# Kernel tuning notes

Measured on AMD Instinct MI355X. Metric: run time of the kernel, lower is better.

The kernel has to match this reference:

```python
import jax, jax.numpy as jnp
import numpy as np

B, N1, N2 = 16, 196, 196
C1, C2, H, O = 768, 768, 512, 128


def setup_inputs() -> dict:
    key = jax.random.key(0)
    k1, k2, kw1, kw2, kwp, kbp = jax.random.split(key, 6)
    x1 = jax.random.normal(k1, (B, N1, C1), dtype=jnp.float32)
    x2 = jax.random.normal(k2, (B, N2, C2), dtype=jnp.float32)
    # kaiming-uniform-ish init scale
    W1 = jax.random.uniform(kw1, (C1, H), dtype=jnp.float32, minval=-1, maxval=1) * np.sqrt(3.0 / C1)
    W2 = jax.random.uniform(kw2, (C2, H), dtype=jnp.float32, minval=-1, maxval=1) * np.sqrt(3.0 / C2)
    Wp = jax.random.uniform(kwp, (H, O), dtype=jnp.float32, minval=-1, maxval=1) * np.sqrt(3.0 / H)
    bp = jax.random.uniform(kbp, (O,), dtype=jnp.float32, minval=-1, maxval=1) * (1.0 / np.sqrt(H))
    return {"x1": x1, "x2": x2, "W1": W1, "W2": W2, "Wp": Wp, "bp": bp}


def reference(x1, x2, W1, W2, Wp, bp):
    # x1: [B,N1,C1], x2: [B,N2,C2]
    h1 = jax.nn.relu(jnp.einsum('bnc,ch->bnh', x1, W1))  # [B,N1,H]
    h2 = jax.nn.relu(jnp.einsum('bmc,ch->bmh', x2, W2))  # [B,N2,H]
    # Original: ((h1[:,:,None,:] * h2[:,None,:,:]) @ Wp + bp).sum(dim=(1,2)).
    # Mathematically identical fused form: sum_{i,j} h1[b,i,h]*h2[b,j,h]
    #   = (sum_i h1)[b,h] * (sum_j h2)[b,h]; bias accumulates N1*N2 times.
    s = h1.sum(axis=1) * h2.sum(axis=1)                   # [B,H]
    return jnp.einsum('bh,ho->bo', s, Wp) + bp * (N1 * N2)
```

## Files before the change

kernel.cpp:

```cpp
#include <hip/hip_runtime.h>
#include <hip/hip_bf16.h>


#define NB 16
#define NROW 196
#define KC_ 768
#define HH 512
#define OO 128

using short8 = __attribute__((ext_vector_type(8))) short;
using f32x16 = __attribute__((ext_vector_type(16))) float;

__device__ __forceinline__ short2 pk2bf(float a, float b) {
    __hip_bfloat162 h = __float22bfloat162_rn(make_float2(a, b));
    union { __hip_bfloat162 h; short2 s; } u; u.h = h;
    return u.s;
}

__global__ __launch_bounds__(512, 1)
void gemm_relu_rowsum(const float* __restrict__ x1, const float* __restrict__ x2,
                      const float* __restrict__ W1, const float* __restrict__ W2,
                      float* __restrict__ sbuf) {
    __shared__ unsigned short Alds[2][8 * 128 * 8];
    __shared__ unsigned short Blds[2][8 * 128 * 8];
    __shared__ float psum[16 * 32];

    const int bid = blockIdx.x;
    const int p  = bid & 31;
    const int tt = bid >> 5;
    const int branch = p >> 4;
    const int b      = p & 15;
    const int ht = tt >> 1;
    const int mh = tt & 1;
    const int c0 = ht * 128;

    const float* __restrict__ x = branch ? x2 : x1;
    const float* __restrict__ W = branch ? W2 : W1;

    const int t  = threadIdx.x;
    const int rn = t & 127;
    const int kg = t >> 7;

    const int r_abs = mh * 128 + rn;
    const bool valid = r_abs < NROW;
    const float* xrow  = x + (b * NROW + (valid ? r_abs : 0)) * KC_ + kg * 16;
    const float* Wbase = W + c0 + rn;

    float4 av[4];
    float  bv[2][8];

    auto load_stage = [&](int kc) {
        const int k0 = kc * 64;
        if (valid) {
#pragma unroll
            for (int i = 0; i < 4; ++i)
                av[i] = *(const float4*)(xrow + k0 + 4 * i);
        } else {
#pragma unroll
            for (int i = 0; i < 4; ++i) av[i] = make_float4(0.f, 0.f, 0.f, 0.f);
        }
#pragma unroll
        for (int u = 0; u < 2; ++u)
#pragma unroll
            for (int j = 0; j < 8; ++j)
                bv[u][j] = Wbase[(k0 + (kg + 4 * u) * 8 + j) * HH];
    };

    auto write_stage = [&](int buf) {
        short8 w0, w1, y0, y1;
        short2 s;
        s = pk2bf(av[0].x, av[0].y); w0[0] = s.x; w0[1] = s.y;
        s = pk2bf(av[0].z, av[0].w); w0[2] = s.x; w0[3] = s.y;
        s = pk2bf(av[1].x, av[1].y); w0[4] = s.x; w0[5] = s.y;
        s = pk2bf(av[1].z, av[1].w); w0[6] = s.x; w0[7] = s.y;
        s = pk2bf(av[2].x, av[2].y); w1[0] = s.x; w1[1] = s.y;
        s = pk2bf(av[2].z, av[2].w); w1[2] = s.x; w1[3] = s.y;
        s = pk2bf(av[3].x, av[3].y); w1[4] = s.x; w1[5] = s.y;
        s = pk2bf(av[3].z, av[3].w); w1[6] = s.x; w1[7] = s.y;
#pragma unroll
        for (int j = 0; j < 4; ++j) {
            s = pk2bf(bv[0][2 * j], bv[0][2 * j + 1]); y0[2 * j] = s.x; y0[2 * j + 1] = s.y;
            s = pk2bf(bv[1][2 * j], bv[1][2 * j + 1]); y1[2 * j] = s.x; y1[2 * j + 1] = s.y;
        }
        *(short8*)&Alds[buf][((2 * kg + 0) * 128 + rn) * 8] = w0;
        *(short8*)&Alds[buf][((2 * kg + 1) * 128 + rn) * 8] = w1;
        *(short8*)&Blds[buf][((kg + 0) * 128 + rn) * 8] = y0;
        *(short8*)&Blds[buf][((kg + 4) * 128 + rn) * 8] = y1;
    };

    const int w  = t >> 6;
    const int l  = t & 63;
    const int m  = l & 31;
    const int q  = l >> 5;
    const int sp = w & 1;
    const int mp = w >> 1;
    const int aoff = (mp * 32 + m) * 8;
    const int boff = (sp * 64 + m) * 8;

    f32x16 acc0 = {}, acc1 = {};

    load_stage(0);
    write_stage(0);
    load_stage(1);
    __syncthreads();

#pragma unroll 1
    for (int kc = 0; kc < 12; ++kc) {
        const int pb = kc & 1;
#pragma unroll
        for (int ks = 0; ks < 4; ++ks) {
            const int base = (ks * 2 + q) * 1024;
            short8 af = *(const short8*)&Alds[pb][base + aoff];
            short8 b0 = *(const short8*)&Blds[pb][base + boff];
            short8 b1 = *(const short8*)&Blds[pb][base + boff + 256];
            acc0 = __builtin_amdgcn_mfma_f32_32x32x16_bf16(af, b0, acc0, 0, 0, 0);
            acc1 = __builtin_amdgcn_mfma_f32_32x32x16_bf16(af, b1, acc1, 0, 0, 0);
        }
        if (kc < 11) write_stage(1 - pb);
        if (kc < 10) load_stage(kc + 2);
        __syncthreads();
    }

    float cs0 = 0.f, cs1 = 0.f;
#pragma unroll
    for (int r = 0; r < 16; ++r) {
        cs0 += fmaxf(acc0[r], 0.f);
        cs1 += fmaxf(acc1[r], 0.f);
    }
    cs0 += __shfl_xor(cs0, 32);
    cs1 += __shfl_xor(cs1, 32);
    if (l < 32) {
        psum[((sp * 2 + 0) * 4 + mp) * 32 + l] = cs0;
        psum[((sp * 2 + 1) * 4 + mp) * 32 + l] = cs1;
    }
    __syncthreads();
    if (t < 128) {
        const int ct = t >> 5;
        const int cl = t & 31;
        float v = 0.f;
#pragma unroll
        for (int mp2 = 0; mp2 < 4; ++mp2)
            v += psum[(ct * 4 + mp2) * 32 + cl];
        sbuf[((branch * 2 + mh) * NB + b) * HH + c0 + t] = v;
    }
}

__global__ __launch_bounds__(512)
void proj_kernel(const float* __restrict__ sbuf, const float* __restrict__ Wp,
                 const float* __restrict__ bp, float* __restrict__ out) {
    __shared__ float spl[HH];
    __shared__ float red[4][OO];
    const int b = blockIdx.x, t = threadIdx.x;
    {
        const float s1 = sbuf[(0 * NB + b) * HH + t] + sbuf[(1 * NB + b) * HH + t];
        const float s2 = sbuf[(2 * NB + b) * HH + t] + sbuf[(3 * NB + b) * HH + t];
        spl[t] = s1 * s2;
    }
    __syncthreads();
    const int to = t & 127, hq = t >> 7;
    float acc = 0.f;
#pragma unroll 8
    for (int h = hq * 128; h < hq * 128 + 128; ++h)
        acc += spl[h] * Wp[h * OO + to];
    red[hq][to] = acc;
    __syncthreads();
    if (t < OO)
        out[b * OO + t] = red[0][t] + red[1][t] + red[2][t] + red[3][t]
                        + bp[t] * 38416.0f;
}

extern "C" void kernel_launch(void* const* d_in, const int* in_sizes, int n_in,
                              void* d_out, int out_size, void* d_ws, size_t ws_size,
                              hipStream_t stream) {
    const float* x1 = (const float*)d_in[0];
    const float* x2 = (const float*)d_in[1];
    const float* W1 = (const float*)d_in[2];
    const float* W2 = (const float*)d_in[3];
    const float* Wp = (const float*)d_in[4];
    const float* bp = (const float*)d_in[5];
    float* sbuf = (float*)d_ws;

    gemm_relu_rowsum<<<256, 512, 0, stream>>>(x1, x2, W1, W2, sbuf);
    proj_kernel<<<NB, 512, 0, stream>>>(sbuf, Wp, bp, (float*)d_out);
}
```

Before: 100.9 us.

## Pre-tile weights to bf16 in a prepass and coalesce x loads with padded LDS

Adds a prepass kernel that converts W1/W2 to bf16 and writes them in the exact tiled layout the GEMM stages into LDS, so the main kernel reads weights with one 16-byte load per chunk instead of strided scalar fp32 loads. The x loads are reorganized so 16 lanes cover a contiguous row segment, which coalesces global reads. LDS rows are padded from 128 to 129 entries to reduce bank conflicts. The cost is an extra kernel launch plus a weight conversion pass on every call, and the change relies on workspace space at a fixed offset.

```diff
diff --git a/kernel.cpp b/kernel.cpp
--- a/kernel.cpp
+++ b/kernel.cpp
@@ -8,6 +8,7 @@
 #define HH 512
 #define OO 128
 
+using short4v = __attribute__((ext_vector_type(4))) short;
 using short8 = __attribute__((ext_vector_type(8))) short;
 using f32x16 = __attribute__((ext_vector_type(16))) float;
 
@@ -17,12 +18,40 @@
     return u.s;
 }
 
+__global__ __launch_bounds__(256)
+void w_tile(const float* __restrict__ W1, const float* __restrict__ W2,
+            unsigned short* __restrict__ Wt) {
+    const int bb = blockIdx.x;
+    const int branch = bb / 48;
+    const int rem = bb % 48;
+    const int ht = rem / 12;
+    const int kc = rem % 12;
+    const float* __restrict__ W = branch ? W2 : W1;
+    unsigned short* __restrict__ out = Wt + (size_t)bb * 8192;
+    const int t = threadIdx.x;
+#pragma unroll
+    for (int i = 0; i < 4; ++i) {
+        const int u = i * 256 + t;
+        const int p = u >> 7, col = u & 127;
+        const float* src = W + (kc * 64 + p * 8) * HH + ht * 128 + col;
+        float f[8];
+#pragma unroll
+        for (int j = 0; j < 8; ++j) f[j] = src[j * HH];
+        short8 v; short2 s;
+#pragma unroll
+        for (int j = 0; j < 4; ++j) {
+            s = pk2bf(f[2 * j], f[2 * j + 1]); v[2 * j] = s.x; v[2 * j + 1] = s.y;
+        }
+        *(short8*)(out + u * 8) = v;
+    }
+}
+
 __global__ __launch_bounds__(512, 1)
 void gemm_relu_rowsum(const float* __restrict__ x1, const float* __restrict__ x2,
-                      const float* __restrict__ W1, const float* __restrict__ W2,
+                      const unsigned short* __restrict__ Wt,
                       float* __restrict__ sbuf) {
-    __shared__ unsigned short Alds[2][8 * 128 * 8];
-    __shared__ unsigned short Blds[2][8 * 128 * 8];
+    __shared__ unsigned short Alds[2][8 * 129 * 8];
+    __shared__ unsigned short Blds[2][8 * 129 * 8];
     __shared__ float psum[16 * 32];
 
     const int bid = blockIdx.x;
@@ -32,60 +61,46 @@
     const int b      = p & 15;
     const int ht = tt >> 1;
     const int mh = tt & 1;
-    const int c0 = ht * 128;
 
     const float* __restrict__ x = branch ? x2 : x1;
-    const float* __restrict__ W = branch ? W2 : W1;
-
-    const int t  = threadIdx.x;
-    const int rn = t & 127;
-    const int kg = t >> 7;
-
-    const int r_abs = mh * 128 + rn;
-    const bool valid = r_abs < NROW;
-    const float* xrow  = x + (b * NROW + (valid ? r_abs : 0)) * KC_ + kg * 16;
-    const float* Wbase = W + c0 + rn;
+    const unsigned short* __restrict__ Wtb = Wt + (size_t)((branch * 4 + ht) * 12) * 8192;
+
+    const int t   = threadIdx.x;
+    const int l16 = t & 15;
+    const int rg  = t >> 4;
+    const float* xbase = x + (b * NROW + mh * 128) * KC_ + l16 * 4;
+
+    const int bp0 = t >> 7,          bc0 = t & 127;
+    const int bp1 = (t + 512) >> 7,  bc1 = t & 127;
 
     float4 av[4];
-    float  bv[2][8];
+    short8 bva, bvb;
 
     auto load_stage = [&](int kc) {
-        const int k0 = kc * 64;
-        if (valid) {
-#pragma unroll
-            for (int i = 0; i < 4; ++i)
-                av[i] = *(const float4*)(xrow + k0 + 4 * i);
-        } else {
-#pragma unroll
-            for (int i = 0; i < 4; ++i) av[i] = make_float4(0.f, 0.f, 0.f, 0.f);
-        }
-#pragma unroll
-        for (int u = 0; u < 2; ++u)
-#pragma unroll
-            for (int j = 0; j < 8; ++j)
-                bv[u][j] = Wbase[(k0 + (kg + 4 * u) * 8 + j) * HH];
+#pragma unroll
+        for (int r = 0; r < 4; ++r) {
+            const int row = rg + 32 * r;
+            if (mh * 128 + row < NROW)
+                av[r] = *(const float4*)(xbase + row * KC_ + kc * 64);
+            else
+                av[r] = make_float4(0.f, 0.f, 0.f, 0.f);
+        }
+        const unsigned short* wc = Wtb + kc * 8192;
+        bva = *(const short8*)(wc + bp0 * 1024 + bc0 * 8);
+        bvb = *(const short8*)(wc + bp1 * 1024 + bc1 * 8);
     };
 
     auto write_stage = [&](int buf) {
-        short8 w0, w1, y0, y1;
-        short2 s;
-        s = pk2bf(av[0].x, av[0].y); w0[0] = s.x; w0[1] = s.y;
-        s = pk2bf(av[0].z, av[0].w); w0[2] = s.x; w0[3] = s.y;
-        s = pk2bf(av[1].x, av[1].y); w0[4] = s.x; w0[5] = s.y;
-        s = pk2bf(av[1].z, av[1].w); w0[6] = s.x; w0[7] = s.y;
-        s = pk2bf(av[2].x, av[2].y); w1[0] = s.x; w1[1] = s.y;
-        s = pk2bf(av[2].z, av[2].w); w1[2] = s.x; w1[3] = s.y;
-        s = pk2bf(av[3].x, av[3].y); w1[4] = s.x; w1[5] = s.y;
-        s = pk2bf(av[3].z, av[3].w); w1[6] = s.x; w1[7] = s.y;
-#pragma unroll
-        for (int j = 0; j < 4; ++j) {
-            s = pk2bf(bv[0][2 * j], bv[0][2 * j + 1]); y0[2 * j] = s.x; y0[2 * j + 1] = s.y;
-            s = pk2bf(bv[1][2 * j], bv[1][2 * j + 1]); y1[2 * j] = s.x; y1[2 * j + 1] = s.y;
-        }
-        *(short8*)&Alds[buf][((2 * kg + 0) * 128 + rn) * 8] = w0;
-        *(short8*)&Alds[buf][((2 * kg + 1) * 128 + rn) * 8] = w1;
-        *(short8*)&Blds[buf][((kg + 0) * 128 + rn) * 8] = y0;
-        *(short8*)&Blds[buf][((kg + 4) * 128 + rn) * 8] = y1;
+#pragma unroll
+        for (int r = 0; r < 4; ++r) {
+            short4v sv; short2 s;
+            s = pk2bf(av[r].x, av[r].y); sv[0] = s.x; sv[1] = s.y;
+            s = pk2bf(av[r].z, av[r].w); sv[2] = s.x; sv[3] = s.y;
+            const int row = rg + 32 * r;
+            *(short4v*)&Alds[buf][((l16 >> 1) * 129 + row) * 8 + (l16 & 1) * 4] = sv;
+        }
+        *(short8*)&Blds[buf][(bp0 * 129 + bc0) * 8] = bva;
+        *(short8*)&Blds[buf][(bp1 * 129 + bc1) * 8] = bvb;
     };
 
     const int w  = t >> 6;
@@ -109,7 +124,7 @@
         const int pb = kc & 1;
 #pragma unroll
         for (int ks = 0; ks < 4; ++ks) {
-            const int base = (ks * 2 + q) * 1024;
+            const int base = (ks * 2 + q) * 129 * 8;
             short8 af = *(const short8*)&Alds[pb][base + aoff];
             short8 b0 = *(const short8*)&Blds[pb][base + boff];
             short8 b1 = *(const short8*)&Blds[pb][base + boff + 256];
@@ -141,7 +156,7 @@
 #pragma unroll
         for (int mp2 = 0; mp2 < 4; ++mp2)
             v += psum[(ct * 4 + mp2) * 32 + cl];
-        sbuf[((branch * 2 + mh) * NB + b) * HH + c0 + t] = v;
+        sbuf[((branch * 2 + mh) * NB + b) * HH + ht * 128 + t] = v;
     }
 }
 
@@ -179,7 +194,9 @@
     const float* Wp = (const float*)d_in[4];
     const float* bp = (const float*)d_in[5];
     float* sbuf = (float*)d_ws;
-
-    gemm_relu_rowsum<<<256, 512, 0, stream>>>(x1, x2, W1, W2, sbuf);
+    unsigned short* Wt = (unsigned short*)((char*)d_ws + 131072);
+
+    w_tile<<<96, 256, 0, stream>>>(W1, W2, Wt);
+    gemm_relu_rowsum<<<256, 512, 0, stream>>>(x1, x2, Wt, sbuf);
     proj_kernel<<<NB, 512, 0, stream>>>(sbuf, Wp, bp, (float*)d_out);
 }
```

New measurement: 94.07 us. 1.07x faster.
